# Optimization experiments

Hardware: AMD Instinct MI355X
Metric: run time of the kernel (lower is better)

The kernel has to match this reference:

```python
import jax, jax.numpy as jnp
import numpy as np

EPS = 1e-6
ROPE_THETA = 1000000.0
SPAN_LENGTHS = [700, 300, 600, 448]
L, D, H, HK, DH, FF = 2, 2048, 16, 8, 128, 8192


def _rmsnorm(x, w):
    var = jnp.mean(jnp.square(x), axis=-1, keepdims=True)
    return x * jax.lax.rsqrt(var + EPS) * w


def _rotate_half(x):
    x1, x2 = jnp.split(x, 2, axis=-1)
    return jnp.concatenate([-x2, x1], axis=-1)


def setup_inputs() -> dict:
    key = jax.random.key(0)
    ks = jax.random.split(key, 8)
    s = 0.02  # init scale
    seg = np.repeat(np.arange(len(SPAN_LENGTHS), dtype=np.int32), SPAN_LENGTHS)
    pos = np.concatenate([np.arange(n, dtype=np.int32) for n in SPAN_LENGTHS])
    T = seg.shape[0]
    return {
        "hidden_states": jax.random.normal(ks[0], (T, D), jnp.float32),
        "ln1_w": jnp.ones((L, D), jnp.float32),
        "ln2_w": jnp.ones((L, D), jnp.float32),
        "wq": jax.random.normal(ks[1], (L, D, H * DH), jnp.float32) * s,
        "wk": jax.random.normal(ks[2], (L, D, HK * DH), jnp.float32) * s,
        "wv": jax.random.normal(ks[3], (L, D, HK * DH), jnp.float32) * s,
        "wo": jax.random.normal(ks[4], (L, H * DH, D), jnp.float32) * s,
        "qn_w": jnp.ones((L, DH), jnp.float32),
        "kn_w": jnp.ones((L, DH), jnp.float32),
        "wg": jax.random.normal(ks[5], (L, D, FF), jnp.float32) * s,
        "wu": jax.random.normal(ks[6], (L, D, FF), jnp.float32) * s,
        "wd": jax.random.normal(ks[7], (L, FF, D), jnp.float32) * s,
        "final_norm_w": jnp.ones((D,), jnp.float32),
        "segment_ids": jnp.asarray(seg),
        "position_ids": jnp.asarray(pos),
    }


def reference(hidden_states, ln1_w, ln2_w, wq, wk, wv, wo, qn_w, kn_w, wg, wu, wd, final_norm_w, segment_ids, position_ids):
    T = hidden_states.shape[0]
    # rotary tables from per-request positions (positions reset per span)
    inv_freq = 1.0 / (ROPE_THETA ** (jnp.arange(0, DH, 2, dtype=jnp.float32) / DH))
    freqs = position_ids.astype(jnp.float32)[:, None] * inv_freq  # [T, DH/2]
    emb = jnp.concatenate([freqs, freqs], axis=-1)                # [T, DH]
    cos = jnp.cos(emb)[:, None, :]
    sin = jnp.sin(emb)[:, None, :]
    # ragged causal mask: attend only within the same request span, causally
    tok = jnp.arange(T)
    mask = (segment_ids[:, None] == segment_ids[None, :]) & (tok[:, None] >= tok[None, :])
    neg = jnp.finfo(hidden_states.dtype).min
    scale = 1.0 / np.sqrt(DH)

    x = hidden_states
    for l in range(L):
        h = _rmsnorm(x, ln1_w[l])
        q = (h @ wq[l]).reshape(T, H, DH)
        k = (h @ wk[l]).reshape(T, HK, DH)
        v = (h @ wv[l]).reshape(T, HK, DH)
        q = _rmsnorm(q, qn_w[l])  # Qwen3 per-head q/k RMSNorm
        k = _rmsnorm(k, kn_w[l])
        q = q * cos + _rotate_half(q) * sin
        k = k * cos + _rotate_half(k) * sin
        rep = H // HK  # GQA
        k = jnp.repeat(k, rep, axis=1)
        v = jnp.repeat(v, rep, axis=1)
        scores = jnp.einsum('thd,shd->hts', q, k) * scale  # [H, T, T]
        scores = jnp.where(mask[None], scores, neg)
        attn = jax.nn.softmax(scores, axis=-1)
        o = jnp.einsum('hts,shd->thd', attn, v).reshape(T, H * DH)
        x = x + o @ wo[l]
        h = _rmsnorm(x, ln2_w[l])
        x = x + (jax.nn.silu(h @ wg[l]) * (h @ wu[l])) @ wd[l]
    return _rmsnorm(x, final_norm_w)
```

## Files before the change

### kernel.cpp

```cpp
#include <hip/hip_runtime.h>
#include <stdint.h>

#define T_SEQ 2048
#define DMODEL 2048
#define NH 16
#define NKV 8
#define DHEAD 128
#define DFF 8192

typedef float f32x4 __attribute__((ext_vector_type(4)));
typedef float f32x2 __attribute__((ext_vector_type(2)));
typedef __bf16 bf16x8 __attribute__((ext_vector_type(8)));
typedef unsigned short ushort_t;

typedef __attribute__((address_space(1))) void gvoid;
typedef __attribute__((address_space(3))) void lvoid;

__device__ inline unsigned short f2bf(float f) {
  unsigned int u = __float_as_uint(f);
  u += 0x7fffu + ((u >> 16) & 1u);
  return (unsigned short)(u >> 16);
}
__device__ inline float bf2f(unsigned short h) {
  return __uint_as_float(((unsigned int)h) << 16);
}

__device__ inline void gload_lds16(const void* g, void* l) {
  __builtin_amdgcn_global_load_lds((gvoid*)g, (lvoid*)l, 16, 0, 0);
}

template <typename TIN>
__global__ __launch_bounds__(256) void k_transpose_bf16(const TIN* __restrict__ in,
                                                        ushort_t* __restrict__ out,
                                                        int R, int C, int rmode) {
  __shared__ float tile[64 * 72];
  int tid = threadIdx.x;
  int r0 = blockIdx.y * 64, c0 = blockIdx.x * 64;
  int rl = tid >> 4;
  int cc = tid & 15;
#pragma unroll
  for (int i = 0; i < 4; ++i) {
    int row = rl + i * 16;
    const TIN* src = in + (size_t)(r0 + row) * C + c0 + cc * 4;
    float v0, v1, v2, v3;
    if constexpr (sizeof(TIN) == 4) {
      f32x4 v = *(const f32x4*)src;
      v0 = v.x; v1 = v.y; v2 = v.z; v3 = v.w;
    } else {
      ushort4 v = *(const ushort4*)src;
      v0 = bf2f(v.x); v1 = bf2f(v.y); v2 = bf2f(v.z); v3 = bf2f(v.w);
    }
    int chunk = cc ^ (row & 15);
    f32x4 t = {v0, v1, v2, v3};
    *(f32x4*)&tile[row * 72 + chunk * 4] = t;
  }
  __syncthreads();
#pragma unroll
  for (int i = 0; i < 4; ++i) {
    int nrow = rl + i * 16;
    int k4 = cc * 4;
    ushort4 o;
    {
      int k = k4 + 0;
      o.x = f2bf(tile[k * 72 + (((nrow >> 2) ^ (k & 15)) << 2) + (nrow & 3)]);
      k = k4 + 1;
      o.y = f2bf(tile[k * 72 + (((nrow >> 2) ^ (k & 15)) << 2) + (nrow & 3)]);
      k = k4 + 2;
      o.z = f2bf(tile[k * 72 + (((nrow >> 2) ^ (k & 15)) << 2) + (nrow & 3)]);
      k = k4 + 3;
      o.w = f2bf(tile[k * 72 + (((nrow >> 2) ^ (k & 15)) << 2) + (nrow & 3)]);
    }
    int n = c0 + nrow;
    int orow = n;
    if (rmode == 1) orow = ((n >> 4) << 5) + (n & 15);
    else if (rmode == 2) orow = ((n >> 4) << 5) + 16 + (n & 15);
    *(ushort4*)(out + (size_t)orow * R + r0 + k4) = o;
  }
}

template <int BF16OUT>
__global__ __launch_bounds__(256) void k_rmsnorm(const float* __restrict__ X,
                                                 const float* __restrict__ W,
                                                 void* __restrict__ OUT) {
  int row = blockIdx.x, tid = threadIdx.x;
  const float* xr = X + (size_t)row * DMODEL;
  f32x4 x0 = *(const f32x4*)(xr + tid * 4);
  f32x4 x1 = *(const f32x4*)(xr + 1024 + tid * 4);
  float ss = x0.x * x0.x + x0.y * x0.y + x0.z * x0.z + x0.w * x0.w +
             x1.x * x1.x + x1.y * x1.y + x1.z * x1.z + x1.w * x1.w;
#pragma unroll
  for (int o = 1; o < 64; o <<= 1) ss += __shfl_xor(ss, o, 64);
  __shared__ float red[4];
  int w = tid >> 6;
  if ((tid & 63) == 0) red[w] = ss;
  __syncthreads();
  float tot = red[0] + red[1] + red[2] + red[3];
  float sc = rsqrtf(tot / (float)DMODEL + 1e-6f);
  f32x4 w0 = *(const f32x4*)(W + tid * 4);
  f32x4 w1 = *(const f32x4*)(W + 1024 + tid * 4);
  if constexpr (BF16OUT) {
    ushort_t* o = (ushort_t*)OUT + (size_t)row * DMODEL;
    ushort4 a, b;
    a.x = f2bf(x0.x * sc * w0.x); a.y = f2bf(x0.y * sc * w0.y);
    a.z = f2bf(x0.z * sc * w0.z); a.w = f2bf(x0.w * sc * w0.w);
    b.x = f2bf(x1.x * sc * w1.x); b.y = f2bf(x1.y * sc * w1.y);
    b.z = f2bf(x1.z * sc * w1.z); b.w = f2bf(x1.w * sc * w1.w);
    *(ushort4*)(o + tid * 4) = a;
    *(ushort4*)(o + 1024 + tid * 4) = b;
  } else {
    float* o = (float*)OUT + (size_t)row * DMODEL;
    f32x4 a = {x0.x * sc * w0.x, x0.y * sc * w0.y, x0.z * sc * w0.z, x0.w * sc * w0.w};
    f32x4 b = {x1.x * sc * w1.x, x1.y * sc * w1.y, x1.z * sc * w1.z, x1.w * sc * w1.w};
    *(f32x4*)(o + tid * 4) = a;
    *(f32x4*)(o + 1024 + tid * 4) = b;
  }
}

template <int NZ, int WRITEH>
__global__ __launch_bounds__(512) void k_redln(const ushort_t* __restrict__ P,
                                               const float* __restrict__ RES,
                                               const float* __restrict__ W,
                                               float* __restrict__ OUT,
                                               ushort_t* __restrict__ HB) {
  int row = blockIdx.x, tid = threadIdx.x;
  size_t base = (size_t)row * DMODEL + tid * 4;
  f32x4 v = *(const f32x4*)(RES + base);
#pragma unroll
  for (int z = 0; z < NZ; ++z) {
    ushort4 t = *(const ushort4*)(P + (size_t)z * T_SEQ * DMODEL + base);
    v.x += bf2f(t.x); v.y += bf2f(t.y); v.z += bf2f(t.z); v.w += bf2f(t.w);
  }
  *(f32x4*)(OUT + base) = v;
  if constexpr (WRITEH) {
    float ss = v.x * v.x + v.y * v.y + v.z * v.z + v.w * v.w;
#pragma unroll
    for (int o = 1; o < 64; o <<= 1) ss += __shfl_xor(ss, o, 64);
    __shared__ float red[8];
    if ((tid & 63) == 0) red[tid >> 6] = ss;
    __syncthreads();
    float tot = 0.f;
#pragma unroll
    for (int i = 0; i < 8; ++i) tot += red[i];
    float sc = rsqrtf(tot / (float)DMODEL + 1e-6f);
    f32x4 wv = *(const f32x4*)(W + tid * 4);
    ushort4 h;
    h.x = f2bf(v.x * sc * wv.x); h.y = f2bf(v.y * sc * wv.y);
    h.z = f2bf(v.z * sc * wv.z); h.w = f2bf(v.w * sc * wv.w);
    *(ushort4*)(HB + base) = h;
  }
}

#define EPI_STOREB 3
#define EPI_GLU 5

#define LOADB(dst, bs, rbase)                                                  \
  {                                                                            \
    _Pragma("unroll") for (int ks = 0; ks < 2; ++ks)                           \
        _Pragma("unroll") for (int ni = 0; ni < 2; ++ni)                       \
            dst[ks][ni] = *(const bf16x8*)((bs) +                              \
                (((rbase) + ni * 16 + lr) << 6) +                              \
                ((((ks << 2) + lg) ^ (lr & 7)) << 3));                         \
  }

#define MFMA_Q(q, B)                                                           \
  {                                                                            \
    _Pragma("unroll") for (int ks = 0; ks < 2; ++ks)                           \
        _Pragma("unroll") for (int mi = 0; mi < 4; ++mi)                       \
            _Pragma("unroll") for (int ni = 0; ni < 2; ++ni)                   \
                acc[mi][(q) * 2 + ni] =                                        \
                    __builtin_amdgcn_mfma_f32_16x16x32_bf16(                   \
                        af[ks][mi], B[ks][ni], acc[mi][(q) * 2 + ni], 0, 0, 0); \
  }

template <int LAST>
__device__ __forceinline__ void g256_iter(
    const ushort_t* __restrict__ as, const ushort_t* __restrict__ bsA,
    const ushort_t* __restrict__ bsB, ushort_t* __restrict__ nA,
    ushort_t* __restrict__ nB, const ushort_t* __restrict__ an,
    const ushort_t* __restrict__ bn, size_t rs, int slds, int lr, int lg,
    f32x4 (&acc)[4][8]) {
  bf16x8 af[2][4], b0[2][2], b1[2][2];
#pragma unroll
  for (int ks = 0; ks < 2; ++ks)
#pragma unroll
    for (int mi = 0; mi < 4; ++mi)
      af[ks][mi] = *(const bf16x8*)(as + ((mi * 16 + lr) << 6) +
                                    ((((ks << 2) + lg) ^ (lr & 7)) << 3));
  LOADB(b0, bsA, 0);
  if constexpr (!LAST) {
    gload_lds16(an, nA + slds);
    gload_lds16(an + rs, nA + 4096 + slds);
    gload_lds16(an + 2 * rs, nA + 8192 + slds);
    gload_lds16(an + 3 * rs, nA + 12288 + slds);
    gload_lds16(bn, nB + slds);
    gload_lds16(bn + rs, nB + 4096 + slds);
    gload_lds16(bn + 2 * rs, nB + 8192 + slds);
    gload_lds16(bn + 3 * rs, nB + 12288 + slds);
  }
  LOADB(b1, bsA, 32);
  asm volatile("s_waitcnt lgkmcnt(4)" ::: "memory");
  __builtin_amdgcn_sched_barrier(0);
  __builtin_amdgcn_s_setprio(1);
  MFMA_Q(0, b0);
  __builtin_amdgcn_s_setprio(0);
  LOADB(b0, bsB, 0);
  asm volatile("s_waitcnt lgkmcnt(4)" ::: "memory");
  __builtin_amdgcn_sched_barrier(0);
  __builtin_amdgcn_s_setprio(1);
  MFMA_Q(1, b1);
  __builtin_amdgcn_s_setprio(0);
  LOADB(b1, bsB, 32);
  asm volatile("s_waitcnt lgkmcnt(4)" ::: "memory");
  __builtin_amdgcn_sched_barrier(0);
  __builtin_amdgcn_s_setprio(1);
  MFMA_Q(2, b0);
  __builtin_amdgcn_s_setprio(0);
  asm volatile("s_waitcnt lgkmcnt(0)" ::: "memory");
  __builtin_amdgcn_sched_barrier(0);
  __builtin_amdgcn_s_setprio(1);
  MFMA_Q(3, b1);
  __builtin_amdgcn_s_setprio(0);
  if constexpr (!LAST) {
    asm volatile("s_waitcnt vmcnt(0)" ::: "memory");
    __builtin_amdgcn_s_barrier();
  }
}

template <int EPI>
__global__ __launch_bounds__(512, 2) void k_gemm256(
    const ushort_t* __restrict__ A, const ushort_t* __restrict__ BT,
    ushort_t* __restrict__ CB, int N, int Kstride, int Kc, size_t zoff) {
  __shared__ ushort_t lds[65536];
  const int tid = threadIdx.x;
  const int l = tid & 63, wid = tid >> 6;
  const int wm = wid >> 1, wn = wid & 1;
  const int lr = l & 15, lg = l >> 4;
  const int gx = gridDim.x;
  const int nwg = gx * gridDim.y;
  const int bid = blockIdx.x + gx * blockIdx.y;
  const int chunk = nwg >> 3;
  const int x = bid & 7;
  const int local = bid >> 3;
  const int cn = chunk >> 2;
  const int ncx = gx / cn;
  const int m0 = ((x / ncx) * 4 + local / cn) * 256;
  const int n0 = ((x % ncx) * cn + local % cn) * 256;
  const int z = blockIdx.z;
  const int NT = Kc >> 6;

  A += (size_t)z * Kc;
  BT += (size_t)z * Kc;
  CB += (size_t)z * zoff;

  const int srow = tid >> 3;
  const int scs = (tid & 7) ^ (srow & 7);
  const size_t sgoff = (size_t)srow * Kstride + scs * 8;
  const int slds = wid * 512;

  const ushort_t* ga = A + (size_t)m0 * Kstride + sgoff;
  const ushort_t* gb = BT + (size_t)n0 * Kstride + sgoff;
  const size_t rs = (size_t)64 * Kstride;

  f32x4 acc[4][8] = {};

  ushort_t* Ab0 = lds;
  ushort_t* Bb0 = lds + 16384;
  ushort_t* Ab1 = lds + 32768;
  ushort_t* Bb1 = lds + 49152;

  gload_lds16(ga, Ab0 + slds);
  gload_lds16(ga + rs, Ab0 + 4096 + slds);
  gload_lds16(ga + 2 * rs, Ab0 + 8192 + slds);
  gload_lds16(ga + 3 * rs, Ab0 + 12288 + slds);
  gload_lds16(gb, Bb0 + slds);
  gload_lds16(gb + rs, Bb0 + 4096 + slds);
  gload_lds16(gb + 2 * rs, Bb0 + 8192 + slds);
  gload_lds16(gb + 3 * rs, Bb0 + 12288 + slds);
  asm volatile("s_waitcnt vmcnt(0)" ::: "memory");
  __builtin_amdgcn_s_barrier();

  for (int kt = 0; kt < NT - 1; ++kt) {
    const int d = kt & 1;
    const ushort_t* as = (d ? Ab1 : Ab0) + wm * 4096;
    const ushort_t* bsA = (d ? Bb1 : Bb0) + (wn * 2) * 4096;
    ushort_t* nA = d ? Ab0 : Ab1;
    ushort_t* nB = d ? Bb0 : Bb1;
    g256_iter<0>(as, bsA, bsA + 4096, nA, nB, ga + (size_t)(kt + 1) * 64,
                 gb + (size_t)(kt + 1) * 64, rs, slds, lr, lg, acc);
  }
  {
    const int d = (NT - 1) & 1;
    const ushort_t* as = (d ? Ab1 : Ab0) + wm * 4096;
    const ushort_t* bsA = (d ? Bb1 : Bb0) + (wn * 2) * 4096;
    g256_iter<1>(as, bsA, bsA + 4096, nullptr, nullptr, nullptr, nullptr, rs,
                 slds, lr, lg, acc);
  }

  if constexpr (EPI == EPI_GLU) {
#pragma unroll
    for (int mi = 0; mi < 4; ++mi)
#pragma unroll
      for (int ci = 0; ci < 8; ci += 2)
#pragma unroll
        for (int rr = 0; rr < 4; ++rr) {
          int m = m0 + wm * 64 + mi * 16 + lg * 4 + rr;
          int nblk = n0 + wn * 128 + ci * 16;
          int col = ((nblk >> 5) << 4) + lr;
          float gv = acc[mi][ci][rr];
          float uv = acc[mi][ci + 1][rr];
          float s = gv / (1.f + __expf(-gv));
          CB[(size_t)m * 8192 + col] = f2bf(s * uv);
        }
  } else {
#pragma unroll
    for (int mi = 0; mi < 4; ++mi)
#pragma unroll
      for (int ci = 0; ci < 8; ++ci)
#pragma unroll
        for (int rr = 0; rr < 4; ++rr) {
          int m = m0 + wm * 64 + mi * 16 + lg * 4 + rr;
          int n = n0 + wn * 128 + ci * 16 + lr;
          CB[(size_t)m * N + n] = f2bf(acc[mi][ci][rr]);
        }
  }
}

__global__ __launch_bounds__(256) void k_qkv_post(const ushort_t* __restrict__ Q0,
                                                  const ushort_t* __restrict__ Q1,
                                                  const float* __restrict__ QNW,
                                                  const float* __restrict__ KNW,
                                                  const int* __restrict__ POS,
                                                  ushort_t* __restrict__ Qb,
                                                  ushort_t* __restrict__ Kb,
                                                  ushort_t* __restrict__ Vb) {
  int t = blockIdx.x;
  int tid = threadIdx.x;
  int w = tid >> 6, l = tid & 63;
  float pos = (float)POS[t];
  const ushort_t* base0 = Q0 + (size_t)t * 4096;
  const ushort_t* base1 = Q1 + (size_t)t * 4096;
  int i0 = 2 * (l & 31);
  const float K2 = 19.931568569324174f / 64.f;
  float ang0 = pos * exp2f(-(float)i0 * K2);
  float ang1 = pos * exp2f(-(float)(i0 + 1) * K2);
  float cs0 = cosf(ang0), sn0 = sinf(ang0);
  float cs1 = cosf(ang1), sn1 = sinf(ang1);
#pragma unroll
  for (int si = 0; si < 8; ++si) {
    int slot = w + si * 4;
    ushort2 xa = *(const ushort2*)(base0 + slot * 128 + l * 2);
    ushort2 xb = *(const ushort2*)(base1 + slot * 128 + l * 2);
    float v0 = bf2f(xa.x) + bf2f(xb.x), v1 = bf2f(xa.y) + bf2f(xb.y);
    float ss = v0 * v0 + v1 * v1;
#pragma unroll
    for (int o = 1; o < 64; o <<= 1) ss += __shfl_xor(ss, o, 64);
    if (slot < 24) {
      float sc = rsqrtf(ss / 128.f + 1e-6f);
      const float* wn = (slot < 16) ? QNW : KNW;
      f32x2 wv = *(const f32x2*)(wn + l * 2);
      v0 = v0 * sc * wv.x;
      v1 = v1 * sc * wv.y;
      float p0 = __shfl_xor(v0, 32, 64);
      float p1 = __shfl_xor(v1, 32, 64);
      float r0 = (l < 32) ? -p0 : p0;
      float r1 = (l < 32) ? -p1 : p1;
      v0 = v0 * cs0 + r0 * sn0;
      v1 = v1 * cs1 + r1 * sn1;
    }
    ushort2 uv;
    uv.x = f2bf(v0);
    uv.y = f2bf(v1);
    ushort_t* dst;
    if (slot < 16)
      dst = Qb + (size_t)t * 2048 + slot * 128 + l * 2;
    else if (slot < 24)
      dst = Kb + (size_t)t * 1024 + (slot - 16) * 128 + l * 2;
    else
      dst = Vb + (size_t)t * 1024 + (slot - 24) * 128 + l * 2;
    *(ushort2*)dst = uv;
  }
}

__global__ __launch_bounds__(64) void k_flash(const ushort_t* __restrict__ Qb,
                                              const ushort_t* __restrict__ Kb,
                                              const ushort_t* __restrict__ VT,
                                              const int* __restrict__ SEG,
                                              ushort_t* __restrict__ Ob) {
  __shared__ ushort_t Pl[2][16 * 40];
  int l = threadIdx.x;
  int qt = blockIdx.x, kvh = blockIdx.y;
  int q0 = qt * 16;
  int lr = l & 15, lg = l >> 4;
  int h0 = kvh * 2;
  bf16x8 qf0[4], qf1[4];
  {
    const bf16x8* qv = (const bf16x8*)(Qb + (size_t)(q0 + lr) * 2048 + h0 * 128);
#pragma unroll
    for (int kk = 0; kk < 4; ++kk) {
      qf0[kk] = qv[kk * 4 + lg];
      qf1[kk] = qv[16 + kk * 4 + lg];
    }
  }
  int segq[4];
#pragma unroll
  for (int r = 0; r < 4; ++r) segq[r] = SEG[q0 + lg * 4 + r];
  int target = SEG[q0];
  int lo = 0, hi = q0;
  while (lo < hi) {
    int mid = (lo + hi) >> 1;
    if (SEG[mid] < target) lo = mid + 1; else hi = mid;
  }
  int s_start = lo & ~31;
  float mr[2][4], lrun[2][4];
  f32x4 acc[2][8] = {};
#pragma unroll
  for (int h = 0; h < 2; ++h)
#pragma unroll
    for (int r = 0; r < 4; ++r) { mr[h][r] = -1e30f; lrun[h][r] = 0.f; }
  const float scale = 0.08838834764831845f;
  for (int s0 = s_start; s0 < q0 + 16; s0 += 32) {
    int sa = s0 + lr, sb = s0 + 16 + lr;
    int sac = min(sa, T_SEQ - 1), sbc = min(sb, T_SEQ - 1);
    bf16x8 vfr[8];
    int sbase = min(s0 + lg * 8, T_SEQ - 8);
#pragma unroll
    for (int c = 0; c < 8; ++c)
      vfr[c] = *(const bf16x8*)(VT + (size_t)(kvh * 128 + c * 16 + lr) * T_SEQ + sbase);
    f32x4 SA0 = {}, SB0 = {}, SA1 = {}, SB1 = {};
    const bf16x8* ka = (const bf16x8*)(Kb + (size_t)sac * 1024 + kvh * 128);
    const bf16x8* kb_ = (const bf16x8*)(Kb + (size_t)sbc * 1024 + kvh * 128);
#pragma unroll
    for (int kk = 0; kk < 4; ++kk) {
      bf16x8 kaf = ka[kk * 4 + lg];
      bf16x8 kbf = kb_[kk * 4 + lg];
      SA0 = __builtin_amdgcn_mfma_f32_16x16x32_bf16(qf0[kk], kaf, SA0, 0, 0, 0);
      SB0 = __builtin_amdgcn_mfma_f32_16x16x32_bf16(qf0[kk], kbf, SB0, 0, 0, 0);
      SA1 = __builtin_amdgcn_mfma_f32_16x16x32_bf16(qf1[kk], kaf, SA1, 0, 0, 0);
      SB1 = __builtin_amdgcn_mfma_f32_16x16x32_bf16(qf1[kk], kbf, SB1, 0, 0, 0);
    }
    int sga = SEG[sac], sgb = SEG[sbc];
    bool mAv[4], mBv[4];
#pragma unroll
    for (int r = 0; r < 4; ++r) {
      int qrow = q0 + lg * 4 + r;
      mAv[r] = (sa <= qrow) && (sga == segq[r]);
      mBv[r] = (sb <= qrow) && (sgb == segq[r]);
    }
#pragma unroll
    for (int h = 0; h < 2; ++h) {
#pragma unroll
      for (int r = 0; r < 4; ++r) {
        float sva = (h ? SA1[r] : SA0[r]);
        float svb = (h ? SB1[r] : SB0[r]);
        float xa = mAv[r] ? sva * scale : -1e30f;
        float xb = mBv[r] ? svb * scale : -1e30f;
        float mx = fmaxf(xa, xb);
#pragma unroll
        for (int o = 1; o < 16; o <<= 1) mx = fmaxf(mx, __shfl_xor(mx, o, 64));
        float nm = fmaxf(mr[h][r], mx);
        float ea = __expf(xa - nm), eb = __expf(xb - nm);
        float rsum = ea + eb;
#pragma unroll
        for (int o = 1; o < 16; o <<= 1) rsum += __shfl_xor(rsum, o, 64);
        float al = __expf(mr[h][r] - nm);
        lrun[h][r] = lrun[h][r] * al + rsum;
        mr[h][r] = nm;
#pragma unroll
        for (int c = 0; c < 8; ++c) acc[h][c][r] *= al;
        Pl[h][(lg * 4 + r) * 40 + lr] = f2bf(ea);
        Pl[h][(lg * 4 + r) * 40 + 16 + lr] = f2bf(eb);
      }
    }
    asm volatile("s_waitcnt lgkmcnt(0)" ::: "memory");
    bf16x8 pa0 = *(const bf16x8*)&Pl[0][lr * 40 + lg * 8];
    bf16x8 pa1 = *(const bf16x8*)&Pl[1][lr * 40 + lg * 8];
#pragma unroll
    for (int c = 0; c < 8; ++c) {
      acc[0][c] = __builtin_amdgcn_mfma_f32_16x16x32_bf16(pa0, vfr[c], acc[0][c], 0, 0, 0);
      acc[1][c] = __builtin_amdgcn_mfma_f32_16x16x32_bf16(pa1, vfr[c], acc[1][c], 0, 0, 0);
    }
  }
#pragma unroll
  for (int h = 0; h < 2; ++h)
#pragma unroll
    for (int c = 0; c < 8; ++c)
#pragma unroll
      for (int r = 0; r < 4; ++r) {
        float ov = acc[h][c][r] / lrun[h][r];
        Ob[(size_t)(q0 + lg * 4 + r) * 2048 + (h0 + h) * 128 + c * 16 + lr] = f2bf(ov);
      }
}

extern "C" void kernel_launch(void* const* d_in, const int* in_sizes, int n_in,
                              void* d_out, int out_size, void* d_ws, size_t ws_size,
                              hipStream_t stream) {
  const float* hidden = (const float*)d_in[0];
  const float* ln1 = (const float*)d_in[1];
  const float* ln2 = (const float*)d_in[2];
  const float* wq = (const float*)d_in[3];
  const float* wk = (const float*)d_in[4];
  const float* wv = (const float*)d_in[5];
  const float* wo = (const float*)d_in[6];
  const float* qnw = (const float*)d_in[7];
  const float* knw = (const float*)d_in[8];
  const float* wg = (const float*)d_in[9];
  const float* wu = (const float*)d_in[10];
  const float* wd = (const float*)d_in[11];
  const float* fnw = (const float*)d_in[12];
  const int* seg = (const int*)d_in[13];
  const int* pos = (const int*)d_in[14];
  float* out = (float*)d_out;

  char* ws = (char*)d_ws;
  size_t off = 0;
  auto alloc = [&](size_t bytes) {
    char* p = ws + off;
    off += (bytes + 255) & ~(size_t)255;
    return p;
  };
  ushort_t* wT = (ushort_t*)alloc((size_t)2 * DFF * DMODEL * 2);
  ushort_t* hbuf = (ushort_t*)alloc((size_t)T_SEQ * DMODEL * 2);
  ushort_t* qb = (ushort_t*)alloc((size_t)T_SEQ * 2048 * 2);
  ushort_t* kb = (ushort_t*)alloc((size_t)T_SEQ * 1024 * 2);
  ushort_t* vb = (ushort_t*)alloc((size_t)T_SEQ * 1024 * 2);
  ushort_t* vT = (ushort_t*)alloc((size_t)T_SEQ * 1024 * 2);
  ushort_t* ob = (ushort_t*)alloc((size_t)T_SEQ * 2048 * 2);
  ushort_t* qkvp = (ushort_t*)alloc((size_t)2 * T_SEQ * 4096 * 2);
  ushort_t* pbuf = (ushort_t*)alloc((size_t)4 * T_SEQ * DMODEL * 2);
  ushort_t* mbuf = (ushort_t*)alloc((size_t)T_SEQ * DFF * 2);
  (void)ws_size; (void)in_sizes; (void)n_in; (void)out_size;

  dim3 b256(256), b64(64), b512(512);
  k_rmsnorm<1><<<T_SEQ, b256, 0, stream>>>(hidden, ln1, hbuf);

  for (int lyr = 0; lyr < 2; ++lyr) {
    const float* xsrc = (lyr == 0) ? hidden : out;

    const float* wql = wq + (size_t)lyr * DMODEL * 2048;
    const float* wkl = wk + (size_t)lyr * DMODEL * 1024;
    const float* wvl = wv + (size_t)lyr * DMODEL * 1024;
    k_transpose_bf16<float><<<dim3(32, 32), b256, 0, stream>>>(wql, wT, 2048, 2048, 0);
    k_transpose_bf16<float><<<dim3(16, 32), b256, 0, stream>>>(wkl, wT + (size_t)2048 * 2048, 2048, 1024, 0);
    k_transpose_bf16<float><<<dim3(16, 32), b256, 0, stream>>>(wvl, wT + (size_t)3072 * 2048, 2048, 1024, 0);
    k_gemm256<EPI_STOREB><<<dim3(16, 8, 2), b512, 0, stream>>>(
        hbuf, wT, qkvp, 4096, 2048, 1024, (size_t)2048 * 4096);
    k_qkv_post<<<T_SEQ, b256, 0, stream>>>(qkvp, qkvp + (size_t)2048 * 4096,
                                           qnw + (size_t)lyr * 128, knw + (size_t)lyr * 128,
                                           pos, qb, kb, vb);
    k_transpose_bf16<ushort_t><<<dim3(16, 32), b256, 0, stream>>>(vb, vT, 2048, 1024, 0);
    k_flash<<<dim3(T_SEQ / 16, NKV), b64, 0, stream>>>(qb, kb, vT, seg, ob);

    const float* wol = wo + (size_t)lyr * 2048 * DMODEL;
    k_transpose_bf16<float><<<dim3(32, 32), b256, 0, stream>>>(wol, wT, 2048, 2048, 0);
    k_gemm256<EPI_STOREB><<<dim3(8, 8, 4), b512, 0, stream>>>(
        ob, wT, pbuf, 2048, 2048, 512, (size_t)2048 * 2048);
    k_redln<4, 1><<<T_SEQ, b512, 0, stream>>>(pbuf, xsrc,
                                              ln2 + (size_t)lyr * DMODEL, out, hbuf);

    const float* wgl = wg + (size_t)lyr * DMODEL * DFF;
    const float* wul = wu + (size_t)lyr * DMODEL * DFF;
    const float* wdl = wd + (size_t)lyr * DFF * DMODEL;
    k_transpose_bf16<float><<<dim3(128, 32), b256, 0, stream>>>(wgl, wT, 2048, 8192, 1);
    k_transpose_bf16<float><<<dim3(128, 32), b256, 0, stream>>>(wul, wT, 2048, 8192, 2);
    k_gemm256<EPI_GLU><<<dim3(64, 8, 1), b512, 0, stream>>>(
        hbuf, wT, mbuf, 16384, 2048, 2048, 0);
    k_transpose_bf16<float><<<dim3(32, 128), b256, 0, stream>>>(wdl, wT, 8192, 2048, 0);
    k_gemm256<EPI_STOREB><<<dim3(8, 8, 4), b512, 0, stream>>>(
        mbuf, wT, pbuf, 2048, 8192, 2048, (size_t)2048 * 2048);
    if (lyr == 0) {
      k_redln<4, 1><<<T_SEQ, b512, 0, stream>>>(pbuf, out, ln1 + DMODEL, out, hbuf);
    } else {
      k_redln<4, 0><<<T_SEQ, b512, 0, stream>>>(pbuf, out, nullptr, out, nullptr);
    }
  }
  k_rmsnorm<0><<<T_SEQ, b256, 0, stream>>>(out, fnw, out);
}
```

Measured before the change: 826.8 us.

## Split flash attention per head, precompute rope tables, vectorize qkv post, fuse final norm

```diff
diff --git a/kernel.cpp b/kernel.cpp
--- a/kernel.cpp
+++ b/kernel.cpp
@@ -11,6 +11,7 @@
 typedef float f32x4 __attribute__((ext_vector_type(4)));
 typedef float f32x2 __attribute__((ext_vector_type(2)));
 typedef __bf16 bf16x8 __attribute__((ext_vector_type(8)));
+typedef unsigned short ushort8 __attribute__((ext_vector_type(8)));
 typedef unsigned short ushort_t;
 
 typedef __attribute__((address_space(1))) void gvoid;
@@ -130,8 +131,8 @@
     ushort4 t = *(const ushort4*)(P + (size_t)z * T_SEQ * DMODEL + base);
     v.x += bf2f(t.x); v.y += bf2f(t.y); v.z += bf2f(t.z); v.w += bf2f(t.w);
   }
-  *(f32x4*)(OUT + base) = v;
-  if constexpr (WRITEH) {
+  if constexpr (WRITEH != 2) *(f32x4*)(OUT + base) = v;
+  if constexpr (WRITEH >= 1) {
     float ss = v.x * v.x + v.y * v.y + v.z * v.z + v.w * v.w;
 #pragma unroll
     for (int o = 1; o < 64; o <<= 1) ss += __shfl_xor(ss, o, 64);
@@ -143,10 +144,15 @@
     for (int i = 0; i < 8; ++i) tot += red[i];
     float sc = rsqrtf(tot / (float)DMODEL + 1e-6f);
     f32x4 wv = *(const f32x4*)(W + tid * 4);
-    ushort4 h;
-    h.x = f2bf(v.x * sc * wv.x); h.y = f2bf(v.y * sc * wv.y);
-    h.z = f2bf(v.z * sc * wv.z); h.w = f2bf(v.w * sc * wv.w);
-    *(ushort4*)(HB + base) = h;
+    if constexpr (WRITEH == 1) {
+      ushort4 h;
+      h.x = f2bf(v.x * sc * wv.x); h.y = f2bf(v.y * sc * wv.y);
+      h.z = f2bf(v.z * sc * wv.z); h.w = f2bf(v.w * sc * wv.w);
+      *(ushort4*)(HB + base) = h;
+    } else {
+      f32x4 o = {v.x * sc * wv.x, v.y * sc * wv.y, v.z * sc * wv.z, v.w * sc * wv.w};
+      *(f32x4*)(OUT + base) = o;
+    }
   }
 }
 
@@ -325,60 +331,83 @@
   }
 }
 
+__global__ __launch_bounds__(64) void k_ropetab(const int* __restrict__ POS,
+                                                float* __restrict__ CS,
+                                                float* __restrict__ SN) {
+  int t = blockIdx.x, d = threadIdx.x;
+  const float K2 = 19.931568569324174f / 64.f;
+  float ang = (float)POS[t] * exp2f(-(float)d * K2);
+  CS[t * 64 + d] = cosf(ang);
+  SN[t * 64 + d] = sinf(ang);
+}
+
 __global__ __launch_bounds__(256) void k_qkv_post(const ushort_t* __restrict__ Q0,
                                                   const ushort_t* __restrict__ Q1,
                                                   const float* __restrict__ QNW,
                                                   const float* __restrict__ KNW,
-                                                  const int* __restrict__ POS,
+                                                  const float* __restrict__ CS,
+                                                  const float* __restrict__ SN,
                                                   ushort_t* __restrict__ Qb,
                                                   ushort_t* __restrict__ Kb,
                                                   ushort_t* __restrict__ Vb) {
-  int t = blockIdx.x;
-  int tid = threadIdx.x;
-  int w = tid >> 6, l = tid & 63;
-  float pos = (float)POS[t];
-  const ushort_t* base0 = Q0 + (size_t)t * 4096;
-  const ushort_t* base1 = Q1 + (size_t)t * 4096;
-  int i0 = 2 * (l & 31);
-  const float K2 = 19.931568569324174f / 64.f;
-  float ang0 = pos * exp2f(-(float)i0 * K2);
-  float ang1 = pos * exp2f(-(float)(i0 + 1) * K2);
-  float cs0 = cosf(ang0), sn0 = sinf(ang0);
-  float cs1 = cosf(ang1), sn1 = sinf(ang1);
-#pragma unroll
-  for (int si = 0; si < 8; ++si) {
-    int slot = w + si * 4;
-    ushort2 xa = *(const ushort2*)(base0 + slot * 128 + l * 2);
-    ushort2 xb = *(const ushort2*)(base1 + slot * 128 + l * 2);
-    float v0 = bf2f(xa.x) + bf2f(xb.x), v1 = bf2f(xa.y) + bf2f(xb.y);
-    float ss = v0 * v0 + v1 * v1;
-#pragma unroll
-    for (int o = 1; o < 64; o <<= 1) ss += __shfl_xor(ss, o, 64);
-    if (slot < 24) {
-      float sc = rsqrtf(ss / 128.f + 1e-6f);
-      const float* wn = (slot < 16) ? QNW : KNW;
-      f32x2 wv = *(const f32x2*)(wn + l * 2);
-      v0 = v0 * sc * wv.x;
-      v1 = v1 * sc * wv.y;
-      float p0 = __shfl_xor(v0, 32, 64);
-      float p1 = __shfl_xor(v1, 32, 64);
-      float r0 = (l < 32) ? -p0 : p0;
-      float r1 = (l < 32) ? -p1 : p1;
-      v0 = v0 * cs0 + r0 * sn0;
-      v1 = v1 * cs1 + r1 * sn1;
-    }
-    ushort2 uv;
-    uv.x = f2bf(v0);
-    uv.y = f2bf(v1);
-    ushort_t* dst;
-    if (slot < 16)
-      dst = Qb + (size_t)t * 2048 + slot * 128 + l * 2;
-    else if (slot < 24)
-      dst = Kb + (size_t)t * 1024 + (slot - 16) * 128 + l * 2;
-    else
-      dst = Vb + (size_t)t * 1024 + (slot - 24) * 128 + l * 2;
-    *(ushort2*)dst = uv;
-  }
+  int t = blockIdx.x, tid = threadIdx.x;
+  int slot = tid >> 3, sub = tid & 7;
+  int d0 = sub * 16;
+  size_t off = (size_t)t * 4096 + slot * 128 + d0;
+  ushort8 a0 = *(const ushort8*)(Q0 + off);
+  ushort8 a1 = *(const ushort8*)(Q0 + off + 8);
+  ushort8 b0 = *(const ushort8*)(Q1 + off);
+  ushort8 b1 = *(const ushort8*)(Q1 + off + 8);
+  float v[16];
+#pragma unroll
+  for (int e = 0; e < 8; ++e) {
+    v[e] = bf2f(a0[e]) + bf2f(b0[e]);
+    v[8 + e] = bf2f(a1[e]) + bf2f(b1[e]);
+  }
+  float ss = 0.f;
+#pragma unroll
+  for (int e = 0; e < 16; ++e) ss += v[e] * v[e];
+#pragma unroll
+  for (int o = 1; o < 8; o <<= 1) ss += __shfl_xor(ss, o, 64);
+  ushort_t* dst;
+  if (slot < 16) dst = Qb + (size_t)t * 2048 + slot * 128 + d0;
+  else if (slot < 24) dst = Kb + (size_t)t * 1024 + (slot - 16) * 128 + d0;
+  else dst = Vb + (size_t)t * 1024 + (slot - 24) * 128 + d0;
+  ushort8 o0, o1;
+  if (slot < 24) {
+    float sc = rsqrtf(ss * (1.f / 128.f) + 1e-6f);
+    const float* nw = (slot < 16) ? QNW : KNW;
+    float w[16], cs[16], sn[16];
+    int ci = t * 64 + (d0 & 63);
+#pragma unroll
+    for (int i = 0; i < 4; ++i) {
+      *(f32x4*)&w[i * 4] = *(const f32x4*)(nw + d0 + i * 4);
+      *(f32x4*)&cs[i * 4] = *(const f32x4*)(CS + ci + i * 4);
+      *(f32x4*)&sn[i * 4] = *(const f32x4*)(SN + ci + i * 4);
+    }
+#pragma unroll
+    for (int e = 0; e < 16; ++e) v[e] = v[e] * sc * w[e];
+    float o[16];
+#pragma unroll
+    for (int e = 0; e < 16; ++e) {
+      float p = __shfl_xor(v[e], 4, 64);
+      float rot = (sub < 4) ? -p : p;
+      o[e] = v[e] * cs[e] + rot * sn[e];
+    }
+#pragma unroll
+    for (int e = 0; e < 8; ++e) {
+      o0[e] = f2bf(o[e]);
+      o1[e] = f2bf(o[8 + e]);
+    }
+  } else {
+#pragma unroll
+    for (int e = 0; e < 8; ++e) {
+      o0[e] = f2bf(v[e]);
+      o1[e] = f2bf(v[8 + e]);
+    }
+  }
+  *(ushort8*)dst = o0;
+  *(ushort8*)(dst + 8) = o1;
 }
 
 __global__ __launch_bounds__(64) void k_flash(const ushort_t* __restrict__ Qb,
@@ -386,20 +415,17 @@
                                               const ushort_t* __restrict__ VT,
                                               const int* __restrict__ SEG,
                                               ushort_t* __restrict__ Ob) {
-  __shared__ ushort_t Pl[2][16 * 40];
+  __shared__ ushort_t Pl[16 * 40];
   int l = threadIdx.x;
-  int qt = blockIdx.x, kvh = blockIdx.y;
+  int qt = blockIdx.x, h = blockIdx.y;
   int q0 = qt * 16;
   int lr = l & 15, lg = l >> 4;
-  int h0 = kvh * 2;
-  bf16x8 qf0[4], qf1[4];
+  int kvh = h >> 1;
+  bf16x8 qf[4];
   {
-    const bf16x8* qv = (const bf16x8*)(Qb + (size_t)(q0 + lr) * 2048 + h0 * 128);
-#pragma unroll
-    for (int kk = 0; kk < 4; ++kk) {
-      qf0[kk] = qv[kk * 4 + lg];
-      qf1[kk] = qv[16 + kk * 4 + lg];
-    }
+    const bf16x8* qv = (const bf16x8*)(Qb + (size_t)(q0 + lr) * 2048 + h * 128);
+#pragma unroll
+    for (int kk = 0; kk < 4; ++kk) qf[kk] = qv[kk * 4 + lg];
   }
   int segq[4];
 #pragma unroll
@@ -411,12 +437,10 @@
     if (SEG[mid] < target) lo = mid + 1; else hi = mid;
   }
   int s_start = lo & ~31;
-  float mr[2][4], lrun[2][4];
-  f32x4 acc[2][8] = {};
-#pragma unroll
-  for (int h = 0; h < 2; ++h)
-#pragma unroll
-    for (int r = 0; r < 4; ++r) { mr[h][r] = -1e30f; lrun[h][r] = 0.f; }
+  float m_run[4], l_run[4];
+  f32x4 acc[8] = {};
+#pragma unroll
+  for (int r = 0; r < 4; ++r) { m_run[r] = -1e30f; l_run[r] = 0.f; }
   const float scale = 0.08838834764831845f;
   for (int s0 = s_start; s0 < q0 + 16; s0 += 32) {
     int sa = s0 + lr, sb = s0 + 16 + lr;
@@ -426,69 +450,61 @@
 #pragma unroll
     for (int c = 0; c < 8; ++c)
       vfr[c] = *(const bf16x8*)(VT + (size_t)(kvh * 128 + c * 16 + lr) * T_SEQ + sbase);
-    f32x4 SA0 = {}, SB0 = {}, SA1 = {}, SB1 = {};
+    f32x4 SA = {}, SB = {};
     const bf16x8* ka = (const bf16x8*)(Kb + (size_t)sac * 1024 + kvh * 128);
     const bf16x8* kb_ = (const bf16x8*)(Kb + (size_t)sbc * 1024 + kvh * 128);
+    __builtin_amdgcn_s_setprio(1);
 #pragma unroll
     for (int kk = 0; kk < 4; ++kk) {
-      bf16x8 kaf = ka[kk * 4 + lg];
-      bf16x8 kbf = kb_[kk * 4 + lg];
-      SA0 = __builtin_amdgcn_mfma_f32_16x16x32_bf16(qf0[kk], kaf, SA0, 0, 0, 0);
-      SB0 = __builtin_amdgcn_mfma_f32_16x16x32_bf16(qf0[kk], kbf, SB0, 0, 0, 0);
-      SA1 = __builtin_amdgcn_mfma_f32_16x16x32_bf16(qf1[kk], kaf, SA1, 0, 0, 0);
-      SB1 = __builtin_amdgcn_mfma_f32_16x16x32_bf16(qf1[kk], kbf, SB1, 0, 0, 0);
-    }
+      SA = __builtin_amdgcn_mfma_f32_16x16x32_bf16(qf[kk], ka[kk * 4 + lg], SA, 0, 0, 0);
+      SB = __builtin_amdgcn_mfma_f32_16x16x32_bf16(qf[kk], kb_[kk * 4 + lg], SB, 0, 0, 0);
+    }
+    __builtin_amdgcn_s_setprio(0);
     int sga = SEG[sac], sgb = SEG[sbc];
-    bool mAv[4], mBv[4];
+    float al[4], pA[4], pB[4];
 #pragma unroll
     for (int r = 0; r < 4; ++r) {
       int qrow = q0 + lg * 4 + r;
-      mAv[r] = (sa <= qrow) && (sga == segq[r]);
-      mBv[r] = (sb <= qrow) && (sgb == segq[r]);
-    }
-#pragma unroll
-    for (int h = 0; h < 2; ++h) {
-#pragma unroll
-      for (int r = 0; r < 4; ++r) {
-        float sva = (h ? SA1[r] : SA0[r]);
-        float svb = (h ? SB1[r] : SB0[r]);
-        float xa = mAv[r] ? sva * scale : -1e30f;
-        float xb = mBv[r] ? svb * scale : -1e30f;
-        float mx = fmaxf(xa, xb);
-#pragma unroll
-        for (int o = 1; o < 16; o <<= 1) mx = fmaxf(mx, __shfl_xor(mx, o, 64));
-        float nm = fmaxf(mr[h][r], mx);
-        float ea = __expf(xa - nm), eb = __expf(xb - nm);
-        float rsum = ea + eb;
-#pragma unroll
-        for (int o = 1; o < 16; o <<= 1) rsum += __shfl_xor(rsum, o, 64);
-        float al = __expf(mr[h][r] - nm);
-        lrun[h][r] = lrun[h][r] * al + rsum;
-        mr[h][r] = nm;
-#pragma unroll
-        for (int c = 0; c < 8; ++c) acc[h][c][r] *= al;
-        Pl[h][(lg * 4 + r) * 40 + lr] = f2bf(ea);
-        Pl[h][(lg * 4 + r) * 40 + 16 + lr] = f2bf(eb);
-      }
+      float xa = (sa <= qrow && sga == segq[r]) ? SA[r] * scale : -1e30f;
+      float xb = (sb <= qrow && sgb == segq[r]) ? SB[r] * scale : -1e30f;
+      float mx = fmaxf(xa, xb);
+#pragma unroll
+      for (int o = 1; o < 16; o <<= 1) mx = fmaxf(mx, __shfl_xor(mx, o, 64));
+      float nm = fmaxf(m_run[r], mx);
+      float ea = __expf(xa - nm), eb = __expf(xb - nm);
+      float rs = ea + eb;
+#pragma unroll
+      for (int o = 1; o < 16; o <<= 1) rs += __shfl_xor(rs, o, 64);
+      al[r] = __expf(m_run[r] - nm);
+      l_run[r] = l_run[r] * al[r] + rs;
+      m_run[r] = nm;
+      pA[r] = ea;
+      pB[r] = eb;
+    }
+#pragma unroll
+    for (int c = 0; c < 8; ++c)
+#pragma unroll
+      for (int r = 0; r < 4; ++r) acc[c][r] *= al[r];
+#pragma unroll
+    for (int r = 0; r < 4; ++r) {
+      Pl[(lg * 4 + r) * 40 + lr] = f2bf(pA[r]);
+      Pl[(lg * 4 + r) * 40 + 16 + lr] = f2bf(pB[r]);
     }
     asm volatile("s_waitcnt lgkmcnt(0)" ::: "memory");
-    bf16x8 pa0 = *(const bf16x8*)&Pl[0][lr * 40 + lg * 8];
-    bf16x8 pa1 = *(const bf16x8*)&Pl[1][lr * 40 + lg * 8];
-#pragma unroll
-    for (int c = 0; c < 8; ++c) {
-      acc[0][c] = __builtin_amdgcn_mfma_f32_16x16x32_bf16(pa0, vfr[c], acc[0][c], 0, 0, 0);
-      acc[1][c] = __builtin_amdgcn_mfma_f32_16x16x32_bf16(pa1, vfr[c], acc[1][c], 0, 0, 0);
-    }
-  }
-#pragma unroll
-  for (int h = 0; h < 2; ++h)
+    bf16x8 pa = *(const bf16x8*)&Pl[lr * 40 + lg * 8];
+    __builtin_amdgcn_s_setprio(1);
 #pragma unroll
     for (int c = 0; c < 8; ++c)
-#pragma unroll
-      for (int r = 0; r < 4; ++r) {
-        float ov = acc[h][c][r] / lrun[h][r];
-        Ob[(size_t)(q0 + lg * 4 + r) * 2048 + (h0 + h) * 128 + c * 16 + lr] = f2bf(ov);
-      }
+      acc[c] = __builtin_amdgcn_mfma_f32_16x16x32_bf16(pa, vfr[c], acc[c], 0, 0, 0);
+    __builtin_amdgcn_s_setprio(0);
+  }
+#pragma unroll
+  for (int c = 0; c < 8; ++c)
+#pragma unroll
+    for (int r = 0; r < 4; ++r) {
+      float ov = acc[c][r] / l_run[r];
+      Ob[(size_t)(q0 + lg * 4 + r) * 2048 + h * 128 + c * 16 + lr] = f2bf(ov);
+    }
 }
 
 extern "C" void kernel_launch(void* const* d_in, const int* in_sizes, int n_in,
@@ -528,9 +544,12 @@
   ushort_t* qkvp = (ushort_t*)alloc((size_t)2 * T_SEQ * 4096 * 2);
   ushort_t* pbuf = (ushort_t*)alloc((size_t)4 * T_SEQ * DMODEL * 2);
   ushort_t* mbuf = (ushort_t*)alloc((size_t)T_SEQ * DFF * 2);
+  float* cstab = (float*)alloc((size_t)T_SEQ * 64 * 4);
+  float* sntab = (float*)alloc((size_t)T_SEQ * 64 * 4);
   (void)ws_size; (void)in_sizes; (void)n_in; (void)out_size;
 
   dim3 b256(256), b64(64), b512(512);
+  k_ropetab<<<T_SEQ, b64, 0, stream>>>(pos, cstab, sntab);
   k_rmsnorm<1><<<T_SEQ, b256, 0, stream>>>(hidden, ln1, hbuf);
 
   for (int lyr = 0; lyr < 2; ++lyr) {
@@ -546,9 +565,9 @@
         hbuf, wT, qkvp, 4096, 2048, 1024, (size_t)2048 * 4096);
     k_qkv_post<<<T_SEQ, b256, 0, stream>>>(qkvp, qkvp + (size_t)2048 * 4096,
                                            qnw + (size_t)lyr * 128, knw + (size_t)lyr * 128,
-                                           pos, qb, kb, vb);
+                                           cstab, sntab, qb, kb, vb);
     k_transpose_bf16<ushort_t><<<dim3(16, 32), b256, 0, stream>>>(vb, vT, 2048, 1024, 0);
-    k_flash<<<dim3(T_SEQ / 16, NKV), b64, 0, stream>>>(qb, kb, vT, seg, ob);
+    k_flash<<<dim3(T_SEQ / 16, NH), b64, 0, stream>>>(qb, kb, vT, seg, ob);
 
     const float* wol = wo + (size_t)lyr * 2048 * DMODEL;
     k_transpose_bf16<float><<<dim3(32, 32), b256, 0, stream>>>(wol, wT, 2048, 2048, 0);
@@ -570,8 +589,7 @@
     if (lyr == 0) {
       k_redln<4, 1><<<T_SEQ, b512, 0, stream>>>(pbuf, out, ln1 + DMODEL, out, hbuf);
     } else {
-      k_redln<4, 0><<<T_SEQ, b512, 0, stream>>>(pbuf, out, nullptr, out, nullptr);
-    }
-  }
-  k_rmsnorm<0><<<T_SEQ, b256, 0, stream>>>(out, fnw, out);
-}
+      k_redln<4, 2><<<T_SEQ, b512, 0, stream>>>(pbuf, out, fnw, out, nullptr);
+    }
+  }
+}
```

After: 906.1 us. 9.6% more time.
